# Kernel optimization log

Hardware: AMD Instinct MI355X
Metric: run time of the kernel (lower is better)

The kernel has to match this reference:

```python
import jax, jax.numpy as jnp
import numpy as np

M, K, N = 32, 8192, 28672

def setup_inputs() -> dict:
    key = jax.random.key(0)
    k1, k2, k3 = jax.random.split(key, 3)
    act = jax.random.normal(k1, (M, K), dtype=jnp.float16)
    # int8 quantized weight, stored as int8 (spec lists int32 for harness compat)
    weight = jax.random.randint(k2, (K, N), -127, 128, dtype=jnp.int8)
    # per-output-channel dequant scale, small positive values typical of fp8/int8 quant
    scale = (jax.random.uniform(k3, (1, N), dtype=jnp.float32) * 0.01 + 1e-4).astype(jnp.float16)
    return {"act": act, "weight": weight, "scale": scale}

def reference(act, weight, scale):
    # grouped_gemm with single group: out[m,n] = (sum_k act[m,k] * w[k,n]) * scale[n]
    # int8 weight is dequantized inline; accumulate in fp32, emit fp16 like the kernel.
    acc = jnp.einsum("mk,kn->mn", act.astype(jnp.float16), weight.astype(jnp.float16),
                     preferred_element_type=jnp.float32)
    out = acc * scale.astype(jnp.float32)
    return out.astype(jnp.float16)
```

## Files before the change

kernel.cpp:

```cpp
#include <hip/hip_runtime.h>
#include <hip/hip_bf16.h>

#define MM 32
#define KK 8192
#define NN 28672

typedef _Float16 half8   __attribute__((ext_vector_type(8)));
typedef __fp16   fp16x2  __attribute__((ext_vector_type(2)));
typedef float    floatx4 __attribute__((ext_vector_type(4)));

__global__ __launch_bounds__(256) void act_cvt_kernel(
    const float* __restrict__ act, __fp16* __restrict__ act16)
{
    int i = (blockIdx.x * 256 + threadIdx.x) * 4;
    floatx4 v = *(const floatx4*)(act + i);
    fp16x2 lo = __builtin_amdgcn_cvt_pkrtz(v[0], v[1]);
    fp16x2 hi = __builtin_amdgcn_cvt_pkrtz(v[2], v[3]);
    __fp16* o = act16 + i;
    *(fp16x2*)(o)     = lo;
    *(fp16x2*)(o + 2) = hi;
}

template <int KSPLIT>
__global__ __launch_bounds__(256, 6) void gemm_stream_kernel(
    const __fp16*   __restrict__ act16,
    const int*      __restrict__ weight,
    float*          __restrict__ ws)
{
    const int lane = threadIdx.x & 63;
    const int wave = threadIdx.x >> 6;
    const int col  = lane & 15;
    const int quad = lane >> 4;

    const int n0 = blockIdx.x * 64 + wave * 16 + col;
    const int kc = blockIdx.y * (KK / KSPLIT);
    constexpr int NSTEP = (KK / KSPLIT) / 32;

    const int*    wp  = weight + (size_t)(kc + quad * 8) * NN + n0;
    const __fp16* ap0 = act16 + (size_t)col * KK + kc + quad * 8;
    const __fp16* ap1 = ap0 + (size_t)16 * KK;

    floatx4 acc0 = {0.f, 0.f, 0.f, 0.f};
    floatx4 acc1 = {0.f, 0.f, 0.f, 0.f};

    int   wA[8], wB[8];
    half8 aA0, aA1, aB0, aB1;

    auto load_step = [&](int (&w)[8], half8& a0, half8& a1) {
#pragma unroll
        for (int j = 0; j < 8; ++j)
            w[j] = wp[(size_t)j * NN];
        a0 = *(const half8*)ap0;
        a1 = *(const half8*)ap1;
        wp  += (size_t)32 * NN;
        ap0 += 32;
        ap1 += 32;
    };

    auto compute_step = [&](const int (&w)[8], const half8 a0, const half8 a1) {
        half8 b;
#pragma unroll
        for (int j = 0; j < 4; ++j) {
            fp16x2 p = __builtin_amdgcn_cvt_pkrtz((float)w[2 * j],
                                                  (float)w[2 * j + 1]);
            b[2 * j]     = p[0];
            b[2 * j + 1] = p[1];
        }
        acc0 = __builtin_amdgcn_mfma_f32_16x16x32_f16(a0, b, acc0, 0, 0, 0);
        acc1 = __builtin_amdgcn_mfma_f32_16x16x32_f16(a1, b, acc1, 0, 0, 0);
    };

    load_step(wA, aA0, aA1);
#pragma unroll 1
    for (int s = 0; s < NSTEP / 2 - 1; ++s) {
        load_step(wB, aB0, aB1);
        compute_step(wA, aA0, aA1);
        load_step(wA, aA0, aA1);
        compute_step(wB, aB0, aB1);
    }
    load_step(wB, aB0, aB1);
    compute_step(wA, aA0, aA1);
    compute_step(wB, aB0, aB1);

    float* wsb = ws + (size_t)blockIdx.y * MM * NN + blockIdx.x * 64
               + wave * 16 + col;
#pragma unroll
    for (int r = 0; r < 4; ++r) {
        int m0 = quad * 4 + r;
        wsb[(size_t)m0 * NN]        = acc0[r];
        wsb[(size_t)(m0 + 16) * NN] = acc1[r];
    }
}

template <int KSPLIT>
__global__ __launch_bounds__(256) void finalize_kernel(
    const float* __restrict__ ws,
    const float* __restrict__ scale,
    float*       __restrict__ out)
{
    const int n = blockIdx.x * 256 + threadIdx.x;
    const int m = blockIdx.y;
    float sum = 0.f;
#pragma unroll
    for (int c = 0; c < KSPLIT; ++c)
        sum += ws[(size_t)c * MM * NN + (size_t)m * NN + n];
    out[(size_t)m * NN + n] = sum * scale[n];
}

__global__ __launch_bounds__(256) void gemm_direct_kernel(
    const float* __restrict__ act,
    const int*   __restrict__ weight,
    const float* __restrict__ scale,
    float*       __restrict__ out)
{
    const int lane = threadIdx.x & 63;
    const int wave = threadIdx.x >> 6;
    const int col  = lane & 15;
    const int quad = lane >> 4;
    const int n0 = blockIdx.x * 64 + wave * 16 + col;

    floatx4 acc0 = {0.f, 0.f, 0.f, 0.f};
    floatx4 acc1 = {0.f, 0.f, 0.f, 0.f};
    const float* ap0 = act + (size_t)col * KK + quad * 8;
    const float* ap1 = ap0 + (size_t)16 * KK;
    const int* wp = weight + (size_t)(quad * 8) * NN + n0;

    for (int s = 0; s < KK / 32; ++s) {
        floatx4 a0lo = *(const floatx4*)(ap0);
        floatx4 a0hi = *(const floatx4*)(ap0 + 4);
        floatx4 a1lo = *(const floatx4*)(ap1);
        floatx4 a1hi = *(const floatx4*)(ap1 + 4);
        half8 a0, a1, b;
#pragma unroll
        for (int j = 0; j < 4; ++j) {
            a0[j] = (_Float16)a0lo[j]; a0[j + 4] = (_Float16)a0hi[j];
            a1[j] = (_Float16)a1lo[j]; a1[j + 4] = (_Float16)a1hi[j];
        }
#pragma unroll
        for (int j = 0; j < 8; ++j)
            b[j] = (_Float16)wp[(size_t)j * NN];
        acc0 = __builtin_amdgcn_mfma_f32_16x16x32_f16(a0, b, acc0, 0, 0, 0);
        acc1 = __builtin_amdgcn_mfma_f32_16x16x32_f16(a1, b, acc1, 0, 0, 0);
        ap0 += 32; ap1 += 32; wp += (size_t)32 * NN;
    }
    float sc = scale[n0];
#pragma unroll
    for (int r = 0; r < 4; ++r) {
        int m0 = quad * 4 + r;
        out[(size_t)m0 * NN + n0]        = acc0[r] * sc;
        out[(size_t)(m0 + 16) * NN + n0] = acc1[r] * sc;
    }
}

extern "C" void kernel_launch(void* const* d_in, const int* in_sizes, int n_in,
                              void* d_out, int out_size, void* d_ws, size_t ws_size,
                              hipStream_t stream)
{
    const float* act    = (const float*)d_in[0];
    const int*   weight = (const int*)d_in[1];
    const float* scale  = (const float*)d_in[2];
    float*       out    = (float*)d_out;

    constexpr int KSPLIT = 4;
    const size_t partials_bytes = (size_t)KSPLIT * MM * NN * sizeof(float);
    const size_t act16_off      = partials_bytes;
    const size_t need           = act16_off + (size_t)MM * KK * sizeof(__fp16);

    if (ws_size >= need) {
        float*   ws_part = (float*)d_ws;
        __fp16*  act16   = (__fp16*)((char*)d_ws + act16_off);

        act_cvt_kernel<<<MM * KK / (256 * 4), 256, 0, stream>>>(act, act16);

        dim3 grid(NN / 64, KSPLIT);
        gemm_stream_kernel<KSPLIT><<<grid, 256, 0, stream>>>(act16, weight, ws_part);

        dim3 fgrid(NN / 256, MM);
        finalize_kernel<KSPLIT><<<fgrid, 256, 0, stream>>>(ws_part, scale, out);
    } else {
        gemm_direct_kernel<<<NN / 64, 256, 0, stream>>>(act, weight, scale, out);
    }
}
```

Measured before the change: 1.263 ms.

## Repack int32 weights into tiled int8 layout before GEMM each call

```diff
diff --git a/kernel.cpp b/kernel.cpp
--- a/kernel.cpp
+++ b/kernel.cpp
@@ -4,10 +4,14 @@
 #define MM 32
 #define KK 8192
 #define NN 28672
+#define NB_COUNT (NN / 64)
+#define REGION_BYTES (2048 * 64)
 
 typedef _Float16 half8   __attribute__((ext_vector_type(8)));
 typedef __fp16   fp16x2  __attribute__((ext_vector_type(2)));
 typedef float    floatx4 __attribute__((ext_vector_type(4)));
+typedef int      intx4   __attribute__((ext_vector_type(4)));
+typedef unsigned int uintx2 __attribute__((ext_vector_type(2)));
 
 __global__ __launch_bounds__(256) void act_cvt_kernel(
     const float* __restrict__ act, __fp16* __restrict__ act16)
@@ -21,69 +25,119 @@
     *(fp16x2*)(o + 2) = hi;
 }
 
+__global__ __launch_bounds__(256) void repack_kernel(
+    const int* __restrict__ weight, unsigned char* __restrict__ wpack)
+{
+    const int t    = threadIdx.x;
+    const int slot = t & 63;
+    const int kg   = t >> 6;
+    const int n_base = blockIdx.x * 512 + slot * 8;
+    const int k_base = blockIdx.y * 32 + kg * 8;
+
+    const int* rp = weight + (size_t)k_base * NN + n_base;
+    intx4 A[8], B[8];
+#pragma unroll
+    for (int j = 0; j < 8; ++j) {
+        A[j] = *(const intx4*)(rp + (size_t)j * NN);
+        B[j] = *(const intx4*)(rp + (size_t)j * NN + 4);
+    }
+
+    const int kc = k_base >> 11;
+    const int s  = (k_base & 2047) >> 5;
+    const int nb = n_base >> 6;
+    const int wv = (n_base & 63) >> 4;
+    const int c0 = n_base & 15;
+    unsigned char* op = wpack
+        + (((size_t)kc * NB_COUNT + nb) << 17)
+        + (s << 11) + (wv << 9) + (kg << 7) + (c0 << 3);
+
+    int d[16];
+#pragma unroll
+    for (int i = 0; i < 4; ++i) {
+        d[2 * i]      = (A[0][i] & 255) | ((A[1][i] & 255) << 8) |
+                        ((A[2][i] & 255) << 16) | (A[3][i] << 24);
+        d[2 * i + 1]  = (A[4][i] & 255) | ((A[5][i] & 255) << 8) |
+                        ((A[6][i] & 255) << 16) | (A[7][i] << 24);
+        d[2 * i + 8]  = (B[0][i] & 255) | ((B[1][i] & 255) << 8) |
+                        ((B[2][i] & 255) << 16) | (B[3][i] << 24);
+        d[2 * i + 9]  = (B[4][i] & 255) | ((B[5][i] & 255) << 8) |
+                        ((B[6][i] & 255) << 16) | (B[7][i] << 24);
+    }
+#pragma unroll
+    for (int q = 0; q < 4; ++q) {
+        intx4 v = {d[4 * q], d[4 * q + 1], d[4 * q + 2], d[4 * q + 3]};
+        *(intx4*)(op + q * 16) = v;
+    }
+}
+
 template <int KSPLIT>
-__global__ __launch_bounds__(256, 6) void gemm_stream_kernel(
-    const __fp16*   __restrict__ act16,
-    const int*      __restrict__ weight,
-    float*          __restrict__ ws)
+__global__ __launch_bounds__(256) void gemm_pack_kernel(
+    const __fp16*        __restrict__ act16,
+    const unsigned char* __restrict__ wpack,
+    float*               __restrict__ ws)
 {
     const int lane = threadIdx.x & 63;
     const int wave = threadIdx.x >> 6;
     const int col  = lane & 15;
     const int quad = lane >> 4;
 
-    const int n0 = blockIdx.x * 64 + wave * 16 + col;
-    const int kc = blockIdx.y * (KK / KSPLIT);
+    const int nb  = blockIdx.x;
+    const int kcb = blockIdx.y;
+    const int kc  = kcb * (KK / KSPLIT);
     constexpr int NSTEP = (KK / KSPLIT) / 32;
 
-    const int*    wp  = weight + (size_t)(kc + quad * 8) * NN + n0;
+    const unsigned char* wp = wpack
+        + (((size_t)kcb * NB_COUNT + nb) << 17)
+        + (wave << 9) + (lane << 3);
     const __fp16* ap0 = act16 + (size_t)col * KK + kc + quad * 8;
     const __fp16* ap1 = ap0 + (size_t)16 * KK;
 
     floatx4 acc0 = {0.f, 0.f, 0.f, 0.f};
     floatx4 acc1 = {0.f, 0.f, 0.f, 0.f};
 
-    int   wA[8], wB[8];
-    half8 aA0, aA1, aB0, aB1;
-
-    auto load_step = [&](int (&w)[8], half8& a0, half8& a1) {
-#pragma unroll
-        for (int j = 0; j < 8; ++j)
-            w[j] = wp[(size_t)j * NN];
-        a0 = *(const half8*)ap0;
-        a1 = *(const half8*)ap1;
-        wp  += (size_t)32 * NN;
-        ap0 += 32;
-        ap1 += 32;
+    uintx2 wA, wB;
+    half8  aA0, aA1, aB0, aB1;
+
+    auto load_step = [&](int s, uintx2& w, half8& a0, half8& a1) {
+        w  = *(const uintx2*)(wp + (size_t)s * 2048);
+        a0 = *(const half8*)(ap0 + s * 32);
+        a1 = *(const half8*)(ap1 + s * 32);
     };
 
-    auto compute_step = [&](const int (&w)[8], const half8 a0, const half8 a1) {
+    auto compute_step = [&](uintx2 w, const half8 a0, const half8 a1) {
+        const unsigned lo = w[0], hi = w[1];
+        int j0 = (int)(lo << 24) >> 24;
+        int j1 = (int)(lo << 16) >> 24;
+        int j2 = (int)(lo <<  8) >> 24;
+        int j3 = (int)lo >> 24;
+        int j4 = (int)(hi << 24) >> 24;
+        int j5 = (int)(hi << 16) >> 24;
+        int j6 = (int)(hi <<  8) >> 24;
+        int j7 = (int)hi >> 24;
+        fp16x2 p0 = __builtin_amdgcn_cvt_pkrtz((float)j0, (float)j1);
+        fp16x2 p1 = __builtin_amdgcn_cvt_pkrtz((float)j2, (float)j3);
+        fp16x2 p2 = __builtin_amdgcn_cvt_pkrtz((float)j4, (float)j5);
+        fp16x2 p3 = __builtin_amdgcn_cvt_pkrtz((float)j6, (float)j7);
         half8 b;
-#pragma unroll
-        for (int j = 0; j < 4; ++j) {
-            fp16x2 p = __builtin_amdgcn_cvt_pkrtz((float)w[2 * j],
-                                                  (float)w[2 * j + 1]);
-            b[2 * j]     = p[0];
-            b[2 * j + 1] = p[1];
-        }
+        b[0] = p0[0]; b[1] = p0[1]; b[2] = p1[0]; b[3] = p1[1];
+        b[4] = p2[0]; b[5] = p2[1]; b[6] = p3[0]; b[7] = p3[1];
         acc0 = __builtin_amdgcn_mfma_f32_16x16x32_f16(a0, b, acc0, 0, 0, 0);
         acc1 = __builtin_amdgcn_mfma_f32_16x16x32_f16(a1, b, acc1, 0, 0, 0);
     };
 
-    load_step(wA, aA0, aA1);
+    load_step(0, wA, aA0, aA1);
 #pragma unroll 1
     for (int s = 0; s < NSTEP / 2 - 1; ++s) {
-        load_step(wB, aB0, aB1);
+        load_step(2 * s + 1, wB, aB0, aB1);
         compute_step(wA, aA0, aA1);
-        load_step(wA, aA0, aA1);
+        load_step(2 * s + 2, wA, aA0, aA1);
         compute_step(wB, aB0, aB1);
     }
-    load_step(wB, aB0, aB1);
+    load_step(NSTEP - 1, wB, aB0, aB1);
     compute_step(wA, aA0, aA1);
     compute_step(wB, aB0, aB1);
 
-    float* wsb = ws + (size_t)blockIdx.y * MM * NN + blockIdx.x * 64
-               + wave * 16 + col;
+    float* wsb = ws + (size_t)kcb * MM * NN + nb * 64 + wave * 16 + col;
 #pragma unroll
     for (int r = 0; r < 4; ++r) {
         int m0 = quad * 4 + r;
@@ -164,16 +218,21 @@
     constexpr int KSPLIT = 4;
     const size_t partials_bytes = (size_t)KSPLIT * MM * NN * sizeof(float);
     const size_t act16_off      = partials_bytes;
-    const size_t need           = act16_off + (size_t)MM * KK * sizeof(__fp16);
+    const size_t wpack_off      = act16_off + (size_t)MM * KK * sizeof(__fp16);
+    const size_t need           = wpack_off + (size_t)KK * NN;
 
     if (ws_size >= need) {
-        float*   ws_part = (float*)d_ws;
-        __fp16*  act16   = (__fp16*)((char*)d_ws + act16_off);
+        float*         ws_part = (float*)d_ws;
+        __fp16*        act16   = (__fp16*)((char*)d_ws + act16_off);
+        unsigned char* wpack   = (unsigned char*)d_ws + wpack_off;
 
         act_cvt_kernel<<<MM * KK / (256 * 4), 256, 0, stream>>>(act, act16);
 
-        dim3 grid(NN / 64, KSPLIT);
-        gemm_stream_kernel<KSPLIT><<<grid, 256, 0, stream>>>(act16, weight, ws_part);
+        dim3 rgrid(NN / 512, KK / 32);
+        repack_kernel<<<rgrid, 256, 0, stream>>>(weight, wpack);
+
+        dim3 ggrid(NB_COUNT, KSPLIT);
+        gemm_pack_kernel<KSPLIT><<<ggrid, 256, 0, stream>>>(act16, wpack, ws_part);
 
         dim3 fgrid(NN / 256, MM);
         finalize_kernel<KSPLIT><<<fgrid, 256, 0, stream>>>(ws_part, scale, out);
```

Result: slower. 1.343 ms (+6.3%).
